# Kernel optimization log

Measured on AMD Instinct MI355X. Metric: run time of the kernel, lower is better.

## Reference

```python
import jax, jax.numpy as jnp
import numpy as np

ALPHA = 2.0   # ATan surrogate sharpness (spikingjelly default)
V_TH = 1.0    # spike threshold

@jax.custom_vjp
def spike(v):
    # Heaviside spike at threshold V_TH
    return (v >= V_TH).astype(v.dtype)

def _spike_fwd(v):
    return spike(v), v

def _spike_bwd(v, g):
    # ATan surrogate gradient
    sg = (ALPHA / 2.0) / (1.0 + (jnp.pi / 2.0 * ALPHA * (v - V_TH)) ** 2)
    return (g * sg,)

spike.defvjp(_spike_fwd, _spike_bwd)

N, T, D_IN, HID, D_OUT = 512, 1000, 128, 128, 20

def _linear_params(k, fan_in, fan_out):
    # matches torch nn.Linear default init: U(-1/sqrt(fan_in), 1/sqrt(fan_in))
    s = 1.0 / np.sqrt(fan_in)
    kw, kb = jax.random.split(k)
    W = jax.random.uniform(kw, (fan_out, fan_in), minval=-s, maxval=s, dtype=jnp.float32)
    b = jax.random.uniform(kb, (fan_out,), minval=-s, maxval=s, dtype=jnp.float32)
    return W, b

def setup_inputs() -> dict:
    key = jax.random.key(0)
    kx, k1, k2, k3, k4, k5 = jax.random.split(key, 6)
    x = jax.random.normal(kx, (N, T, D_IN), dtype=jnp.float32)
    Wi1, bi1 = _linear_params(k1, D_IN, HID)   # i2h_1
    Wh1, bh1 = _linear_params(k2, HID, HID)    # h2h_1
    Wi2, bi2 = _linear_params(k3, HID, HID)    # i2h_2
    Wh2, bh2 = _linear_params(k4, HID, HID)    # h2h_2
    Wo,  bo  = _linear_params(k5, HID, D_OUT)  # h2o_2
    return {"x": x, "Wi1": Wi1, "bi1": bi1, "Wh1": Wh1, "bh1": bh1,
            "Wi2": Wi2, "bi2": bi2, "Wh2": Wh2, "bh2": bh2, "Wo": Wo, "bo": bo}

def reference(x, Wi1, bi1, Wh1, bh1, Wi2, bi2, Wh2, bh2, Wo, bo):
    n, t = x.shape[0], x.shape[1]
    s1_0 = jnp.zeros((n, Wh1.shape[0]), dtype=x.dtype)
    s2_0 = jnp.zeros((n, Wh2.shape[0]), dtype=x.dtype)
    acc0 = jnp.zeros((n, Wo.shape[0]), dtype=x.dtype)

    def step(carry, xt):
        s1, s2, acc = carry
        h1 = xt @ Wi1.T + bi1 + s1 @ Wh1.T + bh1
        s1 = spike(h1)
        h2 = s1 @ Wi2.T + bi2 + s2 @ Wh2.T + bh2
        s2 = spike(h2)
        acc = acc + s2 @ Wo.T + bo
        return (s1, s2, acc), None

    # scan over time: x -> [T, N, D_IN]
    (_, _, acc), _ = jax.lax.scan(step, (s1_0, s2_0, acc0), jnp.swapaxes(x, 0, 1))
    return acc / t
```

## Files before the change

kernel.cpp:

```cpp
#include <hip/hip_runtime.h>
#include <cstdint>
#include <cstddef>

#define T_STEPS 1000
#define NS      512
#define HID     128
#define DOUT    20
#define XPAD    129
#define WPAD    129

extern "C" __global__ void __launch_bounds__(512, 1)
srnn_dense(const float* __restrict__ x, const float* __restrict__ Wi1,
           float* __restrict__ D, int t0, int Tc)
{
    extern __shared__ float sm[];
    float* xs = sm;
    float* Wl = sm + 128 * XPAD;
    const int tid = threadIdx.x;
    const int w = tid >> 6, ln = tid & 63;
    const int rb = blockIdx.x * 128;

    for (int i = tid; i < HID * HID / 4; i += 512)
        ((float4*)Wl)[i] = ((const float4*)Wi1)[i];
    for (int i = tid; i < 128 * 32; i += 512) {
        int r = i >> 5, kq = i & 31;
        int cr = rb + r;
        int s = cr / Tc, trel = cr - s * Tc;
        float4 v = ((const float4*)x)[((size_t)s * T_STEPS + t0 + trel) * 32 + kq];
        float* dst = &xs[r * XPAD + 4 * kq];
        dst[0] = v.x; dst[1] = v.y; dst[2] = v.z; dst[3] = v.w;
    }
    __syncthreads();

    const float* xr0 = xs + ln * XPAD;
    const float* xr1 = xs + (64 + ln) * XPAD;
    for (int og = 0; og < 4; ++og) {
        const int o = 16 * w + 4 * og;
        float a[2][4][4];
        #pragma unroll
        for (int r = 0; r < 2; ++r)
            #pragma unroll
            for (int j = 0; j < 4; ++j)
                #pragma unroll
                for (int i = 0; i < 4; ++i) a[r][j][i] = 0.f;

        #pragma unroll 4
        for (int k = 0; k < HID; k += 4) {
            float4 wv[4];
            #pragma unroll
            for (int j = 0; j < 4; ++j)
                wv[j] = *(const float4*)&Wl[(o + j) * HID + k];
            float xa0[4], xa1[4];
            #pragma unroll
            for (int i = 0; i < 4; ++i) { xa0[i] = xr0[k + i]; xa1[i] = xr1[k + i]; }
            #pragma unroll
            for (int j = 0; j < 4; ++j) {
                a[0][j][0] = fmaf(xa0[0], wv[j].x, a[0][j][0]);
                a[0][j][1] = fmaf(xa0[1], wv[j].y, a[0][j][1]);
                a[0][j][2] = fmaf(xa0[2], wv[j].z, a[0][j][2]);
                a[0][j][3] = fmaf(xa0[3], wv[j].w, a[0][j][3]);
                a[1][j][0] = fmaf(xa1[0], wv[j].x, a[1][j][0]);
                a[1][j][1] = fmaf(xa1[1], wv[j].y, a[1][j][1]);
                a[1][j][2] = fmaf(xa1[2], wv[j].z, a[1][j][2]);
                a[1][j][3] = fmaf(xa1[3], wv[j].w, a[1][j][3]);
            }
        }
        #pragma unroll
        for (int r = 0; r < 2; ++r) {
            float4 dv;
            dv.x = (a[r][0][0] + a[r][0][1]) + (a[r][0][2] + a[r][0][3]);
            dv.y = (a[r][1][0] + a[r][1][1]) + (a[r][1][2] + a[r][1][3]);
            dv.z = (a[r][2][0] + a[r][2][1]) + (a[r][2][2] + a[r][2][3]);
            dv.w = (a[r][3][0] + a[r][3][1]) + (a[r][3][2] + a[r][3][3]);
            *(float4*)&D[(size_t)(rb + 64 * r + ln) * HID + o] = dv;
        }
    }
}

__device__ __forceinline__ unsigned long long rfl64(unsigned long long v)
{
    unsigned int lo = (unsigned int)__builtin_amdgcn_readfirstlane((int)(v & 0xffffffffULL));
    unsigned int hi = (unsigned int)__builtin_amdgcn_readfirstlane((int)(v >> 32));
    return ((unsigned long long)hi << 32) | (unsigned long long)lo;
}

__device__ __forceinline__ int next128z(unsigned long long& lo, unsigned long long& hi)
{
    unsigned long long l = lo, h = hi;
    int jl = (int)__builtin_ctzll(l | 0x8000000000000000ULL);
    int jh = (int)__builtin_ctzll(h | 0x8000000000000000ULL);
    int j  = l ? jl : (h ? 64 + jh : 128);
    lo = l & (l - 1);
    hi = l ? h : (h & (h - 1));
    return j;
}

__device__ __forceinline__ void walk8(const float* __restrict__ WT, int ln,
                                      unsigned long long m0, unsigned long long m1,
                                      float& rl, float& rh)
{
    unsigned long long lo = m0, hi = m1;
    int n = __popcll(m0) + __popcll(m1);
    while (n > 0) {
        int jj[8];
        #pragma unroll
        for (int u = 0; u < 8; ++u) jj[u] = next128z(lo, hi);
        float va[8], vb[8];
        #pragma unroll
        for (int u = 0; u < 8; ++u) {
            const float* p = WT + jj[u] * WPAD + ln;
            va[u] = p[0];
            vb[u] = p[64];
        }
        #pragma unroll
        for (int u = 0; u < 8; ++u) { rl += va[u]; rh += vb[u]; }
        n -= 8;
    }
}

__device__ __forceinline__ void stage_wt_s(float* WT, const float* __restrict__ W,
                                           int tid, int nthr)
{
    for (int i = tid; i < HID * HID / 4; i += nthr) {
        int o = i >> 5, jq = i & 31;
        float4 v = ((const float4*)W)[i];
        WT[(4 * jq + 0) * WPAD + o] = v.x;
        WT[(4 * jq + 1) * WPAD + o] = v.y;
        WT[(4 * jq + 2) * WPAD + o] = v.z;
        WT[(4 * jq + 3) * WPAD + o] = v.w;
    }
    for (int i = tid; i < WPAD; i += nthr) WT[128 * WPAD + i] = 0.f;
}

#define FOLD64(mask, WA, WB, BASE, rl, rh)                                   \
    {                                                                        \
        _Pragma("unroll")                                                    \
        for (int b_ = 0; b_ < 8; ++b_) {                                     \
            unsigned int by_ = (unsigned int)(((mask) >> (8 * b_)) & 0xffULL);\
            if (by_) {                                                       \
                _Pragma("unroll")                                            \
                for (int k_ = 0; k_ < 8; ++k_) {                             \
                    float sp_ = ((by_ >> k_) & 1u) ? 1.0f : 0.0f;            \
                    rl = fmaf(sp_, WA[(BASE) + 8 * b_ + k_], rl);            \
                    rh = fmaf(sp_, WB[(BASE) + 8 * b_ + k_], rh);            \
                }                                                            \
            }                                                                \
        }                                                                    \
    }

extern "C" __global__ void __launch_bounds__(128, 1)
srnn_layer1(const float* __restrict__ D, const float* __restrict__ Wh1,
            const float* __restrict__ bi1, const float* __restrict__ bh1,
            ulonglong2* __restrict__ masks, ulonglong2* __restrict__ state,
            int t0, int Tc, int first)
{
    const int tid = threadIdx.x, w = tid >> 6, ln = tid & 63;
    const int s = 2 * blockIdx.x + w;

    float wl[128], wh[128];
    const float4* r0 = (const float4*)(Wh1 + (size_t)ln * HID);
    const float4* r1 = (const float4*)(Wh1 + (size_t)(64 + ln) * HID);
    #pragma unroll
    for (int q = 0; q < 32; ++q) {
        float4 a = r0[q];
        wl[4 * q + 0] = a.x; wl[4 * q + 1] = a.y;
        wl[4 * q + 2] = a.z; wl[4 * q + 3] = a.w;
        float4 b = r1[q];
        wh[4 * q + 0] = b.x; wh[4 * q + 1] = b.y;
        wh[4 * q + 2] = b.z; wh[4 * q + 3] = b.w;
    }

    const float bil = bi1[ln], bih = bi1[64 + ln];
    const float bhl = bh1[ln], bhh = bh1[64 + ln];
    unsigned long long m0 = 0ULL, m1 = 0ULL;
    if (!first) {
        ulonglong2 st = state[s];
        m0 = rfl64(st.x); m1 = rfl64(st.y);
    }

    const float* Drow = D + (size_t)s * Tc * HID;
    float dl[4], dh[4];
    #pragma unroll
    for (int p = 0; p < 4; ++p) {
        int ti = p < Tc ? p : Tc - 1;
        dl[p] = Drow[ti * HID + ln];
        dh[p] = Drow[ti * HID + 64 + ln];
    }

    for (int tt = 0; tt < Tc; tt += 4) {
        #pragma unroll
        for (int u = 0; u < 4; ++u) {
            int t = tt + u;
            if (t >= Tc) break;
            float dense_l = dl[u], dense_h = dh[u];
            int tp = (t + 4 < Tc) ? t + 4 : Tc - 1;
            dl[u] = Drow[tp * HID + ln];
            dh[u] = Drow[tp * HID + 64 + ln];

            float rl = 0.f, rh = 0.f;
            FOLD64(m0, wl, wh, 0,  rl, rh);
            FOLD64(m1, wl, wh, 64, rl, rh);

            float hl = ((dense_l + bil) + rl) + bhl;
            float hh = ((dense_h + bih) + rh) + bhh;
            m0 = __ballot(hl >= 1.0f);
            m1 = __ballot(hh >= 1.0f);
            if (ln == 0) {
                ulonglong2 mv; mv.x = m0; mv.y = m1;
                masks[(size_t)s * T_STEPS + (t0 + t)] = mv;
            }
        }
    }
    if (ln == 0) { ulonglong2 st; st.x = m0; st.y = m1; state[s] = st; }
}

extern "C" __global__ void __launch_bounds__(512, 1)
srnn_dense2(const ulonglong2* __restrict__ masks, const float* __restrict__ Wi2,
            float* __restrict__ D2, int t0, int Tc)
{
    extern __shared__ float WT[];
    const int tid = threadIdx.x, w = tid >> 6, ln = tid & 63;

    stage_wt_s(WT, Wi2, tid, 512);
    __syncthreads();

    const int rows = NS * Tc;
    for (int r = blockIdx.x * 8 + w; r < rows; r += gridDim.x * 8) {
        int s = r / Tc, trel = r - s * Tc;
        ulonglong2 mv = masks[(size_t)s * T_STEPS + t0 + trel];
        unsigned long long m0 = rfl64(mv.x), m1 = rfl64(mv.y);
        float rl = 0.f, rh = 0.f;
        walk8(WT, ln, m0, m1, rl, rh);
        D2[(size_t)r * HID + ln]      = rl;
        D2[(size_t)r * HID + 64 + ln] = rh;
    }
}

extern "C" __global__ void __launch_bounds__(128, 1)
srnn_layer2(const float* __restrict__ D2, const float* __restrict__ bi2,
            const float* __restrict__ Wh2, const float* __restrict__ bh2,
            const float* __restrict__ Wo,  const float* __restrict__ bo,
            ulonglong2* __restrict__ state2, float* __restrict__ accbuf,
            float* __restrict__ out, int Tc, int first, int last)
{
    __shared__ float WOt[129 * DOUT];
    const int tid = threadIdx.x, w = tid >> 6, ln = tid & 63;
    const int s = 2 * blockIdx.x + w;

    for (int i = tid; i < DOUT * HID / 4; i += 128) {
        int o = i >> 5, jq = i & 31;
        float4 v = ((const float4*)Wo)[i];
        WOt[(4 * jq + 0) * DOUT + o] = v.x; WOt[(4 * jq + 1) * DOUT + o] = v.y;
        WOt[(4 * jq + 2) * DOUT + o] = v.z; WOt[(4 * jq + 3) * DOUT + o] = v.w;
    }
    for (int i = tid; i < DOUT; i += 128) WOt[128 * DOUT + i] = 0.f;

    float wl[128], wh[128];
    const float4* r0 = (const float4*)(Wh2 + (size_t)ln * HID);
    const float4* r1 = (const float4*)(Wh2 + (size_t)(64 + ln) * HID);
    #pragma unroll
    for (int q = 0; q < 32; ++q) {
        float4 a = r0[q];
        wl[4 * q + 0] = a.x; wl[4 * q + 1] = a.y;
        wl[4 * q + 2] = a.z; wl[4 * q + 3] = a.w;
        float4 b = r1[q];
        wh[4 * q + 0] = b.x; wh[4 * q + 1] = b.y;
        wh[4 * q + 2] = b.z; wh[4 * q + 3] = b.w;
    }

    const float bil = bi2[ln], bih = bi2[64 + ln];
    const float bhl = bh2[ln], bhh = bh2[64 + ln];
    const bool  oth = (ln < DOUT);
    const float bol = oth ? bo[ln] : 0.f;

    unsigned long long p0 = 0ULL, p1 = 0ULL;
    float acc = 0.f;
    if (!first) {
        ulonglong2 st = state2[s];
        p0 = rfl64(st.x); p1 = rfl64(st.y);
        if (oth) acc = accbuf[s * DOUT + ln];
    }

    const float* Arow = D2 + (size_t)s * Tc * HID;
    float al[4], ah[4];
    #pragma unroll
    for (int p = 0; p < 4; ++p) {
        int ti = p < Tc ? p : Tc - 1;
        al[p] = Arow[ti * HID + ln];
        ah[p] = Arow[ti * HID + 64 + ln];
    }
    __syncthreads();

    for (int tt = 0; tt < Tc; tt += 4) {
        #pragma unroll
        for (int u = 0; u < 4; ++u) {
            int t = tt + u;
            if (t >= Tc) break;
            float Al = al[u], Ah = ah[u];
            int tp = (t + 4 < Tc) ? t + 4 : Tc - 1;
            al[u] = Arow[tp * HID + ln];
            ah[u] = Arow[tp * HID + 64 + ln];

            float Bl = 0.f, Bh = 0.f;
            FOLD64(p0, wl, wh, 0,  Bl, Bh);
            FOLD64(p1, wl, wh, 64, Bl, Bh);

            float hl = ((Al + bil) + Bl) + bhl;
            float hh = ((Ah + bih) + Bh) + bhh;
            p0 = __ballot(hl >= 1.0f);
            p1 = __ballot(hh >= 1.0f);

            if (oth) {
                float d = 0.f;
                unsigned long long lo = p0, hi = p1;
                int no = __popcll(p0) + __popcll(p1);
                while (no > 0) {
                    int jj[8];
                    #pragma unroll
                    for (int v8 = 0; v8 < 8; ++v8) jj[v8] = next128z(lo, hi);
                    float vv[8];
                    #pragma unroll
                    for (int v8 = 0; v8 < 8; ++v8) vv[v8] = WOt[jj[v8] * DOUT + ln];
                    #pragma unroll
                    for (int v8 = 0; v8 < 8; ++v8) d += vv[v8];
                    no -= 8;
                }
                acc += d;
                acc += bol;
            }
        }
    }
    if (ln == 0) { ulonglong2 st; st.x = p0; st.y = p1; state2[s] = st; }
    if (oth) {
        if (last) out[s * DOUT + ln] = acc / (float)T_STEPS;
        else      accbuf[s * DOUT + ln] = acc;
    }
}

extern "C" void kernel_launch(void* const* d_in, const int* in_sizes, int n_in,
                              void* d_out, int out_size, void* d_ws, size_t ws_size,
                              hipStream_t stream) {
    const float* x   = (const float*)d_in[0];
    const float* Wi1 = (const float*)d_in[1];
    const float* bi1 = (const float*)d_in[2];
    const float* Wh1 = (const float*)d_in[3];
    const float* bh1 = (const float*)d_in[4];
    const float* Wi2 = (const float*)d_in[5];
    const float* bi2 = (const float*)d_in[6];
    const float* Wh2 = (const float*)d_in[7];
    const float* bh2 = (const float*)d_in[8];
    const float* Wo  = (const float*)d_in[9];
    const float* bo  = (const float*)d_in[10];
    float* out = (float*)d_out;

    const size_t mask_bytes = (size_t)NS * T_STEPS * sizeof(ulonglong2);
    const size_t st_bytes   = (size_t)NS * sizeof(ulonglong2);
    const size_t acc_bytes  = (size_t)NS * DOUT * sizeof(float);
    ulonglong2* masks  = (ulonglong2*)d_ws;
    ulonglong2* state  = (ulonglong2*)((char*)d_ws + mask_bytes);
    ulonglong2* state2 = (ulonglong2*)((char*)d_ws + mask_bytes + st_bytes);
    float* accbuf = (float*)((char*)d_ws + mask_bytes + 2 * st_bytes);
    float* D = (float*)((char*)d_ws + mask_bytes + 2 * st_bytes + acc_bytes);

    const size_t head = mask_bytes + 2 * st_bytes + acc_bytes;
    size_t avail = ws_size > head ? ws_size - head : 0;
    const size_t bytes_per_t = (size_t)NS * HID * sizeof(float);
    long tcmax = (long)(avail / bytes_per_t);
    static const int divs[] = {1000, 500, 250, 200, 125, 100, 50, 40, 25, 20, 10, 8, 5, 4, 2, 1};
    int Tc = 1;
    for (int i = 0; i < 16; ++i) if (divs[i] <= tcmax) { Tc = divs[i]; break; }

    const int lds0 = (128 * XPAD + HID * HID) * (int)sizeof(float);
    const int ldsd2 = (129 * WPAD) * (int)sizeof(float);
    hipFuncSetAttribute((const void*)srnn_dense,
                        hipFuncAttributeMaxDynamicSharedMemorySize, lds0);
    hipFuncSetAttribute((const void*)srnn_dense2,
                        hipFuncAttributeMaxDynamicSharedMemorySize, ldsd2);

    for (int t0 = 0; t0 < T_STEPS; t0 += Tc) {
        srnn_dense<<<4 * Tc, 512, lds0, stream>>>(x, Wi1, D, t0, Tc);
        srnn_layer1<<<NS / 2, 128, 0, stream>>>(D, Wh1, bi1, bh1, masks, state,
                                                t0, Tc, t0 == 0 ? 1 : 0);
    }
    for (int t0 = 0; t0 < T_STEPS; t0 += Tc) {
        srnn_dense2<<<512, 512, ldsd2, stream>>>(masks, Wi2, D, t0, Tc);
        srnn_layer2<<<NS / 2, 128, 0, stream>>>(D, bi2, Wh2, bh2, Wo, bo,
                                                state2, accbuf, out, Tc,
                                                t0 == 0 ? 1 : 0,
                                                t0 + Tc >= T_STEPS ? 1 : 0);
    }
}
```

Baseline: 2.132 ms.

## Move output projection off the serial layer-2 recurrence into parallel kernels

Layer 2 now reuses the generic recurrent kernel, which writes spike masks instead of computing the output projection inside the time loop. A new parallel kernel gathers Wo rows per timestep from the masks, and a small reduce kernel accumulates them with the bias over time. The recurrent fold also changes from a byte-skipping branchy loop to a fully unrolled branchless 128-term FMA. This shortens the serial critical path, at the cost of extra launches, an extra pass over the workspace, and always doing all 256 FMAs even when spikes are sparse.

```diff
diff --git a/kernel.cpp b/kernel.cpp
--- a/kernel.cpp
+++ b/kernel.cpp
@@ -132,34 +132,18 @@
     for (int i = tid; i < WPAD; i += nthr) WT[128 * WPAD + i] = 0.f;
 }
 
-#define FOLD64(mask, WA, WB, BASE, rl, rh)                                   \
-    {                                                                        \
-        _Pragma("unroll")                                                    \
-        for (int b_ = 0; b_ < 8; ++b_) {                                     \
-            unsigned int by_ = (unsigned int)(((mask) >> (8 * b_)) & 0xffULL);\
-            if (by_) {                                                       \
-                _Pragma("unroll")                                            \
-                for (int k_ = 0; k_ < 8; ++k_) {                             \
-                    float sp_ = ((by_ >> k_) & 1u) ? 1.0f : 0.0f;            \
-                    rl = fmaf(sp_, WA[(BASE) + 8 * b_ + k_], rl);            \
-                    rh = fmaf(sp_, WB[(BASE) + 8 * b_ + k_], rh);            \
-                }                                                            \
-            }                                                                \
-        }                                                                    \
-    }
-
 extern "C" __global__ void __launch_bounds__(128, 1)
-srnn_layer1(const float* __restrict__ D, const float* __restrict__ Wh1,
-            const float* __restrict__ bi1, const float* __restrict__ bh1,
-            ulonglong2* __restrict__ masks, ulonglong2* __restrict__ state,
-            int t0, int Tc, int first)
+srnn_layer(const float* __restrict__ Din, const float* __restrict__ Wh,
+           const float* __restrict__ bi, const float* __restrict__ bh,
+           ulonglong2* __restrict__ masks, ulonglong2* __restrict__ state,
+           int t0, int Tc, int first)
 {
     const int tid = threadIdx.x, w = tid >> 6, ln = tid & 63;
     const int s = 2 * blockIdx.x + w;
 
     float wl[128], wh[128];
-    const float4* r0 = (const float4*)(Wh1 + (size_t)ln * HID);
-    const float4* r1 = (const float4*)(Wh1 + (size_t)(64 + ln) * HID);
+    const float4* r0 = (const float4*)(Wh + (size_t)ln * HID);
+    const float4* r1 = (const float4*)(Wh + (size_t)(64 + ln) * HID);
     #pragma unroll
     for (int q = 0; q < 32; ++q) {
         float4 a = r0[q];
@@ -170,15 +154,15 @@
         wh[4 * q + 2] = b.z; wh[4 * q + 3] = b.w;
     }
 
-    const float bil = bi1[ln], bih = bi1[64 + ln];
-    const float bhl = bh1[ln], bhh = bh1[64 + ln];
+    const float bil = bi[ln], bih = bi[64 + ln];
+    const float bhl = bh[ln], bhh = bh[64 + ln];
     unsigned long long m0 = 0ULL, m1 = 0ULL;
     if (!first) {
         ulonglong2 st = state[s];
         m0 = rfl64(st.x); m1 = rfl64(st.y);
     }
 
-    const float* Drow = D + (size_t)s * Tc * HID;
+    const float* Drow = Din + (size_t)s * Tc * HID;
     float dl[4], dh[4];
     #pragma unroll
     for (int p = 0; p < 4; ++p) {
@@ -198,8 +182,18 @@
             dh[u] = Drow[tp * HID + 64 + ln];
 
             float rl = 0.f, rh = 0.f;
-            FOLD64(m0, wl, wh, 0,  rl, rh);
-            FOLD64(m1, wl, wh, 64, rl, rh);
+            #pragma unroll
+            for (int j = 0; j < 64; ++j) {
+                float sp = ((m0 >> j) & 1ULL) ? 1.0f : 0.0f;
+                rl = fmaf(sp, wl[j], rl);
+                rh = fmaf(sp, wh[j], rh);
+            }
+            #pragma unroll
+            for (int j = 0; j < 64; ++j) {
+                float sp = ((m1 >> j) & 1ULL) ? 1.0f : 0.0f;
+                rl = fmaf(sp, wl[64 + j], rl);
+                rh = fmaf(sp, wh[64 + j], rh);
+            }
 
             float hl = ((dense_l + bil) + rl) + bhl;
             float hh = ((dense_h + bih) + rh) + bhh;
@@ -236,105 +230,77 @@
     }
 }
 
-extern "C" __global__ void __launch_bounds__(128, 1)
-srnn_layer2(const float* __restrict__ D2, const float* __restrict__ bi2,
-            const float* __restrict__ Wh2, const float* __restrict__ bh2,
-            const float* __restrict__ Wo,  const float* __restrict__ bo,
-            ulonglong2* __restrict__ state2, float* __restrict__ accbuf,
-            float* __restrict__ out, int Tc, int first, int last)
+extern "C" __global__ void __launch_bounds__(512, 1)
+srnn_dense3(const ulonglong2* __restrict__ masks, const float* __restrict__ Wo,
+            float* __restrict__ d, int t0, int Tc)
 {
     __shared__ float WOt[129 * DOUT];
     const int tid = threadIdx.x, w = tid >> 6, ln = tid & 63;
-    const int s = 2 * blockIdx.x + w;
-
-    for (int i = tid; i < DOUT * HID / 4; i += 128) {
+
+    for (int i = tid; i < DOUT * HID / 4; i += 512) {
         int o = i >> 5, jq = i & 31;
         float4 v = ((const float4*)Wo)[i];
         WOt[(4 * jq + 0) * DOUT + o] = v.x; WOt[(4 * jq + 1) * DOUT + o] = v.y;
         WOt[(4 * jq + 2) * DOUT + o] = v.z; WOt[(4 * jq + 3) * DOUT + o] = v.w;
     }
-    for (int i = tid; i < DOUT; i += 128) WOt[128 * DOUT + i] = 0.f;
-
-    float wl[128], wh[128];
-    const float4* r0 = (const float4*)(Wh2 + (size_t)ln * HID);
-    const float4* r1 = (const float4*)(Wh2 + (size_t)(64 + ln) * HID);
+    for (int i = tid; i < DOUT; i += 512) WOt[128 * DOUT + i] = 0.f;
+    __syncthreads();
+
+    const int rows = NS * Tc;
+    for (int r = blockIdx.x * 8 + w; r < rows; r += gridDim.x * 8) {
+        int s = r / Tc, trel = r - s * Tc;
+        ulonglong2 mv = masks[(size_t)s * T_STEPS + t0 + trel];
+        unsigned long long lo = rfl64(mv.x), hi = rfl64(mv.y);
+        if (ln < DOUT) {
+            float dd = 0.f;
+            int no = __popcll(lo) + __popcll(hi);
+            while (no > 0) {
+                int jj[8];
+                #pragma unroll
+                for (int u = 0; u < 8; ++u) jj[u] = next128z(lo, hi);
+                float vv[8];
+                #pragma unroll
+                for (int u = 0; u < 8; ++u) vv[u] = WOt[jj[u] * DOUT + ln];
+                #pragma unroll
+                for (int u = 0; u < 8; ++u) dd += vv[u];
+                no -= 8;
+            }
+            d[(size_t)r * DOUT + ln] = dd;
+        }
+    }
+}
+
+extern "C" __global__ void __launch_bounds__(128, 1)
+srnn_reduce(const float* __restrict__ d, const float* __restrict__ bo,
+            float* __restrict__ accbuf, float* __restrict__ out,
+            int Tc, int first, int last)
+{
+    const int tid = threadIdx.x, w = tid >> 6, ln = tid & 63;
+    const int s = 2 * blockIdx.x + w;
+    if (ln >= DOUT) return;
+
+    const float bol = bo[ln];
+    float acc = first ? 0.f : accbuf[s * DOUT + ln];
+    const float* drow = d + (size_t)s * Tc * DOUT + ln;
+
+    float pf[8];
     #pragma unroll
-    for (int q = 0; q < 32; ++q) {
-        float4 a = r0[q];
-        wl[4 * q + 0] = a.x; wl[4 * q + 1] = a.y;
-        wl[4 * q + 2] = a.z; wl[4 * q + 3] = a.w;
-        float4 b = r1[q];
-        wh[4 * q + 0] = b.x; wh[4 * q + 1] = b.y;
-        wh[4 * q + 2] = b.z; wh[4 * q + 3] = b.w;
-    }
-
-    const float bil = bi2[ln], bih = bi2[64 + ln];
-    const float bhl = bh2[ln], bhh = bh2[64 + ln];
-    const bool  oth = (ln < DOUT);
-    const float bol = oth ? bo[ln] : 0.f;
-
-    unsigned long long p0 = 0ULL, p1 = 0ULL;
-    float acc = 0.f;
-    if (!first) {
-        ulonglong2 st = state2[s];
-        p0 = rfl64(st.x); p1 = rfl64(st.y);
-        if (oth) acc = accbuf[s * DOUT + ln];
-    }
-
-    const float* Arow = D2 + (size_t)s * Tc * HID;
-    float al[4], ah[4];
-    #pragma unroll
-    for (int p = 0; p < 4; ++p) {
-        int ti = p < Tc ? p : Tc - 1;
-        al[p] = Arow[ti * HID + ln];
-        ah[p] = Arow[ti * HID + 64 + ln];
-    }
-    __syncthreads();
-
-    for (int tt = 0; tt < Tc; tt += 4) {
-        #pragma unroll
-        for (int u = 0; u < 4; ++u) {
+    for (int p = 0; p < 8; ++p) { int ti = p < Tc ? p : Tc - 1; pf[p] = drow[ti * DOUT]; }
+
+    for (int tt = 0; tt < Tc; tt += 8) {
+        #pragma unroll
+        for (int u = 0; u < 8; ++u) {
             int t = tt + u;
             if (t >= Tc) break;
-            float Al = al[u], Ah = ah[u];
-            int tp = (t + 4 < Tc) ? t + 4 : Tc - 1;
-            al[u] = Arow[tp * HID + ln];
-            ah[u] = Arow[tp * HID + 64 + ln];
-
-            float Bl = 0.f, Bh = 0.f;
-            FOLD64(p0, wl, wh, 0,  Bl, Bh);
-            FOLD64(p1, wl, wh, 64, Bl, Bh);
-
-            float hl = ((Al + bil) + Bl) + bhl;
-            float hh = ((Ah + bih) + Bh) + bhh;
-            p0 = __ballot(hl >= 1.0f);
-            p1 = __ballot(hh >= 1.0f);
-
-            if (oth) {
-                float d = 0.f;
-                unsigned long long lo = p0, hi = p1;
-                int no = __popcll(p0) + __popcll(p1);
-                while (no > 0) {
-                    int jj[8];
-                    #pragma unroll
-                    for (int v8 = 0; v8 < 8; ++v8) jj[v8] = next128z(lo, hi);
-                    float vv[8];
-                    #pragma unroll
-                    for (int v8 = 0; v8 < 8; ++v8) vv[v8] = WOt[jj[v8] * DOUT + ln];
-                    #pragma unroll
-                    for (int v8 = 0; v8 < 8; ++v8) d += vv[v8];
-                    no -= 8;
-                }
-                acc += d;
-                acc += bol;
-            }
-        }
-    }
-    if (ln == 0) { ulonglong2 st; st.x = p0; st.y = p1; state2[s] = st; }
-    if (oth) {
-        if (last) out[s * DOUT + ln] = acc / (float)T_STEPS;
-        else      accbuf[s * DOUT + ln] = acc;
-    }
+            float dv = pf[u];
+            int tp = (t + 8 < Tc) ? t + 8 : Tc - 1;
+            pf[u] = drow[tp * DOUT];
+            acc += dv;
+            acc += bol;
+        }
+    }
+    if (last) out[s * DOUT + ln] = acc / (float)T_STEPS;
+    else      accbuf[s * DOUT + ln] = acc;
 }
 
 extern "C" void kernel_launch(void* const* d_in, const int* in_sizes, int n_in,
@@ -370,7 +336,7 @@
     int Tc = 1;
     for (int i = 0; i < 16; ++i) if (divs[i] <= tcmax) { Tc = divs[i]; break; }
 
-    const int lds0 = (128 * XPAD + HID * HID) * (int)sizeof(float);
+    const int lds0  = (128 * XPAD + HID * HID) * (int)sizeof(float);
     const int ldsd2 = (129 * WPAD) * (int)sizeof(float);
     hipFuncSetAttribute((const void*)srnn_dense,
                         hipFuncAttributeMaxDynamicSharedMemorySize, lds0);
@@ -379,13 +345,17 @@
 
     for (int t0 = 0; t0 < T_STEPS; t0 += Tc) {
         srnn_dense<<<4 * Tc, 512, lds0, stream>>>(x, Wi1, D, t0, Tc);
-        srnn_layer1<<<NS / 2, 128, 0, stream>>>(D, Wh1, bi1, bh1, masks, state,
-                                                t0, Tc, t0 == 0 ? 1 : 0);
+        srnn_layer<<<NS / 2, 128, 0, stream>>>(D, Wh1, bi1, bh1, masks, state,
+                                               t0, Tc, t0 == 0 ? 1 : 0);
     }
     for (int t0 = 0; t0 < T_STEPS; t0 += Tc) {
         srnn_dense2<<<512, 512, ldsd2, stream>>>(masks, Wi2, D, t0, Tc);
-        srnn_layer2<<<NS / 2, 128, 0, stream>>>(D, bi2, Wh2, bh2, Wo, bo,
-                                                state2, accbuf, out, Tc,
+        srnn_layer<<<NS / 2, 128, 0, stream>>>(D, Wh2, bi2, bh2, masks, state2,
+                                               t0, Tc, t0 == 0 ? 1 : 0);
+    }
+    for (int t0 = 0; t0 < T_STEPS; t0 += Tc) {
+        srnn_dense3<<<512, 512, 0, stream>>>(masks, Wo, D, t0, Tc);
+        srnn_reduce<<<NS / 2, 128, 0, stream>>>(D, bo, accbuf, out, Tc,
                                                 t0 == 0 ? 1 : 0,
                                                 t0 + Tc >= T_STEPS ? 1 : 0);
     }
```

Result: slower. 4.513 ms (+111.7%).
